# Optimization experiments

Hardware: AMD Instinct MI355X
Metric: run time of the kernel (lower is better)

## Reference

```python
import jax, jax.numpy as jnp
import numpy as np

LOG_STD_MAX = 2.0
LOG_STD_MIN = -5.0
N_LAYERS = 10
HID = 512
OBS = 21
ACT = 8
OVERALL = HID * (N_LAYERS + 1)          # 5632
IN_DIM = OBS + OVERALL                   # 5653
OUT_DIM = OVERALL + ACT                  # 5640
BATCH = 8192


def _block_banded_weight(rng):
    # staircase partitions, exactly as layer_init
    in_d = [0, OBS] + [OBS + HID * i for i in range(1, N_LAYERS + 2)]
    out_d = [0] + [HID * i for i in range(1, N_LAYERS + 2)] + [OUT_DIM]
    W = np.zeros((OUT_DIM, IN_DIM), dtype=np.float32)
    for i in range(N_LAYERS + 2):
        r0, r1 = out_d[i], out_d[i + 1]
        c0, c1 = in_d[i], in_d[i + 1]
        fan_in = c1 - c0
        std = np.sqrt(2.0 / fan_in)  # kaiming_normal_ fan_in, gain sqrt(2)
        W[r0:r1, c0:c1] = rng.standard_normal((r1 - r0, c1 - c0)).astype(np.float32) * std
    return jnp.asarray(W)


def setup_inputs() -> dict:
    key = jax.random.key(0)
    k1, k2, k3, k4, k5, k6 = jax.random.split(key, 6)
    rng = np.random.default_rng(0)
    return {
        "obs": jax.random.normal(k1, (BATCH, OBS), dtype=jnp.float32),
        "hidden0": jax.random.uniform(k2, (BATCH, OVERALL), dtype=jnp.float32),
        "prev_mean": jax.random.normal(k3, (BATCH, ACT), dtype=jnp.float32),
        "prev_logstd": jax.random.normal(k4, (BATCH, ACT), dtype=jnp.float32),
        "W_mean": _block_banded_weight(rng),
        "b_mean": jnp.zeros((OUT_DIM,), dtype=jnp.float32),
        "W_logstd": jax.random.normal(k5, (ACT, IN_DIM), dtype=jnp.float32) / np.sqrt(IN_DIM),
        "b_logstd": jax.random.normal(k6, (ACT,), dtype=jnp.float32) * 0.01,
    }


def reference(obs, hidden0, prev_mean, prev_logstd, W_mean, b_mean, W_logstd, b_logstd):
    x = jnp.concatenate([obs, hidden0], axis=1)            # [B, IN_DIM]
    new_x = x @ W_mean.T + b_mean                          # [B, OUT_DIM]
    new_hidden = jax.nn.relu(new_x[:, :-ACT])              # [B, OVERALL]
    new_mean = new_x[:, -ACT:]                             # [B, ACT]
    new_log_std = x @ W_logstd.T + b_logstd                # [B, ACT]
    # outputs come from the PREVIOUS step's (mean, log_std)
    log_std = jnp.tanh(prev_logstd)
    log_std = LOG_STD_MIN + 0.5 * (LOG_STD_MAX - LOG_STD_MIN) * (log_std + 1.0)
    return (prev_mean, log_std, new_hidden, new_mean, new_log_std)
```

## Files before the change

### kernel.cpp

```cpp
#include <hip/hip_runtime.h>
#include <math.h>

typedef unsigned short u16;
typedef unsigned int u32;
typedef __attribute__((ext_vector_type(8))) short short8;
typedef __attribute__((ext_vector_type(4))) float float4v;

#define BATCH   8192
#define OBS     21
#define HID     512
#define NL      10
#define OVERALL 5632
#define IN_DIM  5653
#define ACT     8

#define O_PM   0
#define O_LS   65536
#define O_NH   131072
#define O_NM   (131072 + BATCH*OVERALL)
#define O_NLS  (O_NM + 65536)

#define WSP_TOTAL (10*512*512)
#define WSP_BYTES ((size_t)WSP_TOTAL * 2)

__device__ __forceinline__ u16 f2bf(float f) {
    u32 u = __float_as_uint(f);
    u32 r = (u + 0x7fffu + ((u >> 16) & 1u)) >> 16;
    return (u16)r;
}
__device__ __forceinline__ u32 pkbf(float a, float b) {
    return (u32)f2bf(a) | ((u32)f2bf(b) << 16);
}
__device__ __forceinline__ void gload_lds16(const void* g, void* l) {
    __builtin_amdgcn_global_load_lds(
        (const __attribute__((address_space(1))) char*)g,
        (__attribute__((address_space(3))) char*)l, 16, 0, 0);
}

__global__ __launch_bounds__(256) void k_pack(const float* __restrict__ Wm,
                                              u16* __restrict__ ws) {
    int idx = blockIdx.x * 256 + threadIdx.x;
    if (idx >= WSP_TOTAL) return;
    int z = idx >> 18;
    int rem = idx & 262143;
    int n = rem >> 9, k = rem & 511;
    float v = Wm[(size_t)(512 * (z + 1) + n) * IN_DIM + OBS + 512 * z + k];
    ws[idx] = f2bf(v);
}

#define BM 128
#define BK 32
#define LDA 40
__global__ __launch_bounds__(1024, 4) void k_fused(
        const float* __restrict__ X,
        const float* __restrict__ Wm_raw,
        const u16* __restrict__ Wp,
        const float* __restrict__ Wls_raw,
        const float* __restrict__ b_mean,
        float* __restrict__ out_h,
        float* __restrict__ out_ls,
        float* __restrict__ out_mean,
        int packed) {
    __shared__ __attribute__((aligned(16))) u16 As[BM * LDA];
    __shared__ __attribute__((aligned(16))) u16 Bs[512 * 32];
    __shared__ __attribute__((aligned(16))) u16 Wt[16 * 520];
    u16* Wt2 = (u16*)Bs;

    int t = threadIdx.x;
    int w = t >> 6, lane = t & 63;
    int quad = lane >> 4, r16 = lane & 15;
    int gm = blockIdx.x * BM;
    int z = blockIdx.y;
    bool mainz = (z < 10);
    int wm = (w >> 3) * 64;
    int wn = (w & 7) * 64;

    {
        int n = t >> 7;
        int k4 = (t & 127) * 4;
        const float* wr = Wls_raw + (size_t)n * IN_DIM + OBS + z * 512 + k4;
        u16* dst = &Wt[n * 520 + k4];
        dst[0] = f2bf(wr[0]); dst[1] = f2bf(wr[1]);
        dst[2] = f2bf(wr[2]); dst[3] = f2bf(wr[3]);
        if (!mainz) {
            const float* wr2 = Wm_raw + (size_t)(OVERALL + n) * IN_DIM + OBS + z * 512 + k4;
            u16* d2 = &Wt2[n * 520 + k4];
            d2[0] = f2bf(wr2[0]); d2[1] = f2bf(wr2[1]);
            d2[2] = f2bf(wr2[2]); d2[3] = f2bf(wr2[3]);
        }
    }

    int arow = t >> 3;
    int acol = (t & 7) * 4;
    const float* gA = X + (size_t)(gm + arow) * OVERALL + (size_t)z * 512 + acol;
    float4 areg = *(const float4*)(gA);

    float4v acc[4][4];
#pragma unroll
    for (int i = 0; i < 4; i++)
#pragma unroll
        for (int j = 0; j < 4; j++) acc[i][j] = (float4v)0.f;
    float4v accL = (float4v)0.f;

    for (int it = 0; it < 16; ++it) {
        int k0 = it * BK;
        __syncthreads();
        {
            uint2 p;
            p.x = pkbf(areg.x, areg.y);
            p.y = pkbf(areg.z, areg.w);
            *(uint2*)&As[arow * LDA + acol] = p;
        }
        if (mainz) {
            if (packed) {
#pragma unroll
                for (int i2 = 0; i2 < 2; ++i2) {
                    int base_row = i2 * 256 + w * 16;
                    int row = base_row + (lane >> 2);
                    int slot = lane & 3;
                    int j = (slot - row) & 3;
                    const u16* g = Wp + (size_t)z * 262144 + (size_t)row * 512 + k0 + j * 8;
                    gload_lds16(g, (char*)Bs + base_row * 64);
                }
            } else {
#pragma unroll
                for (int i2 = 0; i2 < 2; ++i2) {
                    int row = i2 * 256 + w * 16 + (lane >> 2);
                    int slot = lane & 3;
                    int j = (slot - row) & 3;
                    const float* g = Wm_raw + (size_t)(512 * (z + 1) + row) * IN_DIM
                                     + OBS + (size_t)z * 512 + k0 + j * 8;
                    uint4 q;
                    q.x = pkbf(g[0], g[1]); q.y = pkbf(g[2], g[3]);
                    q.z = pkbf(g[4], g[5]); q.w = pkbf(g[6], g[7]);
                    *(uint4*)&Bs[row * 32 + slot * 8] = q;
                }
            }
        }
        __syncthreads();
        if (it < 15) areg = *(const float4*)(gA + (it + 1) * BK);

        if (mainz) {
            short8 bfr[4];
#pragma unroll
            for (int j = 0; j < 4; j++) {
                int n = wn + j * 16 + r16;
                int s = (quad + n) & 3;
                bfr[j] = *(const short8*)&Bs[n * 32 + s * 8];
            }
#pragma unroll
            for (int i2 = 0; i2 < 4; i2++) {
                short8 af = *(const short8*)&As[(wm + i2 * 16 + r16) * LDA + quad * 8];
#pragma unroll
                for (int j = 0; j < 4; j++)
                    acc[i2][j] = __builtin_amdgcn_mfma_f32_16x16x32_bf16(af, bfr[j], acc[i2][j], 0, 0, 0);
            }
        }
        if (w < 8) {
            short8 aL = *(const short8*)&As[(w * 16 + r16) * LDA + quad * 8];
            short8 bL = *(const short8*)&Wt[r16 * 520 + k0 + quad * 8];
            accL = __builtin_amdgcn_mfma_f32_16x16x32_bf16(aL, bL, accL, 0, 0, 0);
        } else if (!mainz) {
            short8 aL = *(const short8*)&As[((w - 8) * 16 + r16) * LDA + quad * 8];
            short8 bL = *(const short8*)&Wt2[r16 * 520 + k0 + quad * 8];
            accL = __builtin_amdgcn_mfma_f32_16x16x32_bf16(aL, bL, accL, 0, 0, 0);
        }
    }

    if (mainz) {
        int colblock = (z + 1) * 512;
#pragma unroll
        for (int j = 0; j < 4; j++) {
            int n_loc = wn + j * 16 + r16;
            float bias = b_mean[colblock + n_loc];
#pragma unroll
            for (int i2 = 0; i2 < 4; i2++) {
                int m0 = gm + wm + i2 * 16 + quad * 4;
#pragma unroll
                for (int r = 0; r < 4; r++) {
                    float v = acc[i2][j][r] + bias;
                    out_h[(size_t)(m0 + r) * OVERALL + colblock + n_loc] = fmaxf(v, 0.f);
                }
            }
        }
    }
    if (w < 8) {
        if (r16 < ACT) {
#pragma unroll
            for (int r = 0; r < 4; r++) {
                int row = gm + w * 16 + quad * 4 + r;
                atomicAdd(&out_ls[(size_t)row * ACT + r16], accL[r]);
            }
        }
    } else if (!mainz) {
        if (r16 < ACT) {
            float bias = b_mean[OVERALL + r16];
#pragma unroll
            for (int r = 0; r < 4; r++) {
                int row = gm + (w - 8) * 16 + quad * 4 + r;
                out_mean[(size_t)row * ACT + r16] = accL[r] + bias;
            }
        }
    }
}

#define B0_ROWS 32
__global__ __launch_bounds__(256) void k_block0(const float* __restrict__ obs,
                                                const float* __restrict__ Wm,
                                                const float* __restrict__ b_mean,
                                                float* __restrict__ out_h) {
    __shared__ float w0[OBS * 512];
    __shared__ float bias_s[512];
    __shared__ float obs_s[B0_ROWS * OBS];
    int t = threadIdx.x;
    int b0 = blockIdx.x * B0_ROWS;
    for (int i = t; i < OBS * 512; i += 256) {
        int n = i / OBS, k = i - n * OBS;
        w0[k * 512 + n] = Wm[(size_t)n * IN_DIM + k];
    }
    for (int i = t; i < 512; i += 256) bias_s[i] = b_mean[i];
    for (int i = t; i < B0_ROWS * OBS; i += 256) obs_s[i] = obs[(size_t)b0 * OBS + i];
    __syncthreads();

    int n0 = (t & 127) * 4;
    int rh = t >> 7;
#pragma unroll 4
    for (int r = 0; r < 16; r++) {
        int row = rh * 16 + r;
        float acc0 = bias_s[n0], acc1 = bias_s[n0 + 1];
        float acc2 = bias_s[n0 + 2], acc3 = bias_s[n0 + 3];
#pragma unroll
        for (int k = 0; k < OBS; k++) {
            float xo = obs_s[row * OBS + k];
            const float* wr = &w0[k * 512 + n0];
            acc0 += xo * wr[0]; acc1 += xo * wr[1];
            acc2 += xo * wr[2]; acc3 += xo * wr[3];
        }
        float4 o;
        o.x = fmaxf(acc0, 0.f); o.y = fmaxf(acc1, 0.f);
        o.z = fmaxf(acc2, 0.f); o.w = fmaxf(acc3, 0.f);
        *(float4*)&out_h[(size_t)(b0 + row) * OVERALL + n0] = o;
    }
}

__global__ __launch_bounds__(256) void k_finish(const float* __restrict__ obs,
                                                const float* __restrict__ Wls,
                                                const float* __restrict__ b_logstd,
                                                const float* __restrict__ pm,
                                                const float* __restrict__ pls,
                                                float* __restrict__ o_pm,
                                                float* __restrict__ o_lstd,
                                                float* __restrict__ o_nls) {
    __shared__ float wobs[ACT * OBS];
    __shared__ float bls[ACT];
    int t = threadIdx.x;
    if (t < ACT * OBS) wobs[t] = Wls[(size_t)(t / OBS) * IN_DIM + (t % OBS)];
    if (t < ACT) bls[t] = b_logstd[t];
    __syncthreads();
    int row = blockIdx.x * 256 + t;
    float ob[OBS];
#pragma unroll
    for (int k = 0; k < OBS; k++) ob[k] = obs[(size_t)row * OBS + k];
#pragma unroll
    for (int n = 0; n < ACT; n++) {
        float a = bls[n];
#pragma unroll
        for (int k = 0; k < OBS; k++) a += ob[k] * wobs[n * OBS + k];
        o_nls[(size_t)row * ACT + n] += a;
    }
    float4 p0 = *(const float4*)(pm + (size_t)row * ACT);
    float4 p1 = *(const float4*)(pm + (size_t)row * ACT + 4);
    *(float4*)(o_pm + (size_t)row * ACT) = p0;
    *(float4*)(o_pm + (size_t)row * ACT + 4) = p1;
    float4 l0 = *(const float4*)(pls + (size_t)row * ACT);
    float4 l1 = *(const float4*)(pls + (size_t)row * ACT + 4);
    float4 q0, q1;
    q0.x = -5.f + 3.5f * (tanhf(l0.x) + 1.f);
    q0.y = -5.f + 3.5f * (tanhf(l0.y) + 1.f);
    q0.z = -5.f + 3.5f * (tanhf(l0.z) + 1.f);
    q0.w = -5.f + 3.5f * (tanhf(l0.w) + 1.f);
    q1.x = -5.f + 3.5f * (tanhf(l1.x) + 1.f);
    q1.y = -5.f + 3.5f * (tanhf(l1.y) + 1.f);
    q1.z = -5.f + 3.5f * (tanhf(l1.z) + 1.f);
    q1.w = -5.f + 3.5f * (tanhf(l1.w) + 1.f);
    *(float4*)(o_lstd + (size_t)row * ACT) = q0;
    *(float4*)(o_lstd + (size_t)row * ACT + 4) = q1;
}

extern "C" void kernel_launch(void* const* d_in, const int* in_sizes, int n_in,
                              void* d_out, int out_size, void* d_ws, size_t ws_size,
                              hipStream_t stream) {
    const float* obs         = (const float*)d_in[0];
    const float* hidden0     = (const float*)d_in[1];
    const float* prev_mean   = (const float*)d_in[2];
    const float* prev_logstd = (const float*)d_in[3];
    const float* W_mean      = (const float*)d_in[4];
    const float* b_mean      = (const float*)d_in[5];
    const float* W_logstd    = (const float*)d_in[6];
    const float* b_logstd    = (const float*)d_in[7];

    float* out   = (float*)d_out;
    float* o_pm  = out + O_PM;
    float* o_ls  = out + O_LS;
    float* o_nh  = out + O_NH;
    float* o_nm  = out + O_NM;
    float* o_nls = out + O_NLS;
    u16*   ws    = (u16*)d_ws;

    int packed = (ws != nullptr && ws_size >= WSP_BYTES) ? 1 : 0;

    if (packed) {
        k_pack<<<(WSP_TOTAL + 255) / 256, 256, 0, stream>>>(W_mean, ws);
    }
    hipMemsetAsync(o_nls, 0, (size_t)BATCH * ACT * sizeof(float), stream);
    k_fused<<<dim3(BATCH / BM, NL + 1), 1024, 0, stream>>>(
        hidden0, W_mean, ws, W_logstd, b_mean, o_nh, o_nls, o_nm, packed);
    k_block0<<<BATCH / B0_ROWS, 256, 0, stream>>>(obs, W_mean, b_mean, o_nh);
    k_finish<<<BATCH / 256, 256, 0, stream>>>(obs, W_logstd, b_logstd,
                                              prev_mean, prev_logstd,
                                              o_pm, o_ls, o_nls);
}
```

Measured before the change: 453.8 us.

## Stage whole A tile in LDS once and stream B fragments straight from global

The fused GEMM kernel now uses 64-row blocks of 512 threads. Each block loads its full 64x512 A slab into XOR-swizzled LDS once, with a single barrier, instead of double-staging A and B through LDS every k-step. Each wave reads its B fragments directly from the packed bf16 weights in global/L2 and the log-std weights straight from global memory, which removes the per-iteration barriers. The cost is more blocks, twice the weight re-reads across M tiles, and B loads that depend on cache hits.

```diff
diff --git a/kernel.cpp b/kernel.cpp
--- a/kernel.cpp
+++ b/kernel.cpp
@@ -30,11 +30,6 @@
 }
 __device__ __forceinline__ u32 pkbf(float a, float b) {
     return (u32)f2bf(a) | ((u32)f2bf(b) << 16);
-}
-__device__ __forceinline__ void gload_lds16(const void* g, void* l) {
-    __builtin_amdgcn_global_load_lds(
-        (const __attribute__((address_space(1))) char*)g,
-        (__attribute__((address_space(3))) char*)l, 16, 0, 0);
 }
 
 __global__ __launch_bounds__(256) void k_pack(const float* __restrict__ Wm,
@@ -48,10 +43,8 @@
     ws[idx] = f2bf(v);
 }
 
-#define BM 128
-#define BK 32
-#define LDA 40
-__global__ __launch_bounds__(1024, 4) void k_fused(
+#define BM 64
+__global__ __launch_bounds__(512, 4) void k_fused(
         const float* __restrict__ X,
         const float* __restrict__ Wm_raw,
         const u16* __restrict__ Wp,
@@ -61,144 +54,126 @@
         float* __restrict__ out_ls,
         float* __restrict__ out_mean,
         int packed) {
-    __shared__ __attribute__((aligned(16))) u16 As[BM * LDA];
-    __shared__ __attribute__((aligned(16))) u16 Bs[512 * 32];
-    __shared__ __attribute__((aligned(16))) u16 Wt[16 * 520];
-    u16* Wt2 = (u16*)Bs;
-
-    int t = threadIdx.x;
-    int w = t >> 6, lane = t & 63;
-    int quad = lane >> 4, r16 = lane & 15;
-    int gm = blockIdx.x * BM;
-    int z = blockIdx.y;
-    bool mainz = (z < 10);
-    int wm = (w >> 3) * 64;
-    int wn = (w & 7) * 64;
+    __shared__ __attribute__((aligned(16))) u16 As[64 * 512];
+
+    const int t = threadIdx.x;
+    const int w = t >> 6, lane = t & 63;
+    const int quad = lane >> 4, r16 = lane & 15;
+    const int gm = blockIdx.x * BM;
+    const int z = blockIdx.y;
+    const bool mainz = (z < 10);
 
     {
-        int n = t >> 7;
-        int k4 = (t & 127) * 4;
-        const float* wr = Wls_raw + (size_t)n * IN_DIM + OBS + z * 512 + k4;
-        u16* dst = &Wt[n * 520 + k4];
-        dst[0] = f2bf(wr[0]); dst[1] = f2bf(wr[1]);
-        dst[2] = f2bf(wr[2]); dst[3] = f2bf(wr[3]);
-        if (!mainz) {
-            const float* wr2 = Wm_raw + (size_t)(OVERALL + n) * IN_DIM + OBS + z * 512 + k4;
-            u16* d2 = &Wt2[n * 520 + k4];
-            d2[0] = f2bf(wr2[0]); d2[1] = f2bf(wr2[1]);
-            d2[2] = f2bf(wr2[2]); d2[3] = f2bf(wr2[3]);
-        }
-    }
-
-    int arow = t >> 3;
-    int acol = (t & 7) * 4;
-    const float* gA = X + (size_t)(gm + arow) * OVERALL + (size_t)z * 512 + acol;
-    float4 areg = *(const float4*)(gA);
+        const float* xb = X + (size_t)gm * OVERALL + (size_t)z * 512;
+#pragma unroll
+        for (int u = 0; u < 8; ++u) {
+            int row = u * 8 + w;
+            const float* g = xb + (size_t)row * OVERALL + lane * 8;
+            float4 f0 = *(const float4*)g;
+            float4 f1 = *(const float4*)(g + 4);
+            uint4 p;
+            p.x = pkbf(f0.x, f0.y); p.y = pkbf(f0.z, f0.w);
+            p.z = pkbf(f1.x, f1.y); p.w = pkbf(f1.z, f1.w);
+            *(uint4*)&As[row * 512 + ((lane ^ w) << 3)] = p;
+        }
+    }
+    __syncthreads();
 
     float4v acc[4][4];
 #pragma unroll
-    for (int i = 0; i < 4; i++)
-#pragma unroll
-        for (int j = 0; j < 4; j++) acc[i][j] = (float4v)0.f;
-    float4v accL = (float4v)0.f;
-
+    for (int i = 0; i < 4; ++i)
+#pragma unroll
+        for (int j = 0; j < 4; ++j) acc[i][j] = (float4v)0.f;
+    float4v accE = (float4v)0.f;
+
+    const int n8 = r16 & 7;
+    const u16* bp = Wp + (size_t)z * 262144
+                       + (size_t)(w * 64 + r16) * 512 + quad * 8;
+    const float* gL = Wls_raw + (size_t)n8 * IN_DIM + OBS + z * 512 + quad * 8;
+    const float* gM = Wm_raw + (size_t)(OVERALL + n8) * IN_DIM + OBS + z * 512 + quad * 8;
+
+#pragma unroll 4
     for (int it = 0; it < 16; ++it) {
-        int k0 = it * BK;
-        __syncthreads();
-        {
-            uint2 p;
-            p.x = pkbf(areg.x, areg.y);
-            p.y = pkbf(areg.z, areg.w);
-            *(uint2*)&As[arow * LDA + acol] = p;
+        const int k0 = it * 32;
+        const int phys = ((it * 4 + quad) ^ (r16 & 7)) << 3;
+        short8 a[4];
+#pragma unroll
+        for (int i2 = 0; i2 < 4; ++i2) {
+            int row = i2 * 16 + r16;
+            a[i2] = *(const short8*)&As[row * 512 + phys];
         }
         if (mainz) {
+            short8 b[4];
             if (packed) {
 #pragma unroll
-                for (int i2 = 0; i2 < 2; ++i2) {
-                    int base_row = i2 * 256 + w * 16;
-                    int row = base_row + (lane >> 2);
-                    int slot = lane & 3;
-                    int j = (slot - row) & 3;
-                    const u16* g = Wp + (size_t)z * 262144 + (size_t)row * 512 + k0 + j * 8;
-                    gload_lds16(g, (char*)Bs + base_row * 64);
+                for (int j = 0; j < 4; ++j)
+                    b[j] = *(const short8*)(bp + j * 8192 + k0);
+            } else {
+#pragma unroll
+                for (int j = 0; j < 4; ++j) {
+                    const float* g = Wm_raw
+                        + (size_t)(512 * (z + 1) + w * 64 + j * 16 + r16) * IN_DIM
+                        + OBS + (size_t)z * 512 + k0 + quad * 8;
+                    union { short8 s; uint4 u; } cb;
+                    cb.u.x = pkbf(g[0], g[1]); cb.u.y = pkbf(g[2], g[3]);
+                    cb.u.z = pkbf(g[4], g[5]); cb.u.w = pkbf(g[6], g[7]);
+                    b[j] = cb.s;
                 }
-            } else {
-#pragma unroll
-                for (int i2 = 0; i2 < 2; ++i2) {
-                    int row = i2 * 256 + w * 16 + (lane >> 2);
-                    int slot = lane & 3;
-                    int j = (slot - row) & 3;
-                    const float* g = Wm_raw + (size_t)(512 * (z + 1) + row) * IN_DIM
-                                     + OBS + (size_t)z * 512 + k0 + j * 8;
-                    uint4 q;
-                    q.x = pkbf(g[0], g[1]); q.y = pkbf(g[2], g[3]);
-                    q.z = pkbf(g[4], g[5]); q.w = pkbf(g[6], g[7]);
-                    *(uint4*)&Bs[row * 32 + slot * 8] = q;
-                }
-            }
-        }
-        __syncthreads();
-        if (it < 15) areg = *(const float4*)(gA + (it + 1) * BK);
-
-        if (mainz) {
-            short8 bfr[4];
-#pragma unroll
-            for (int j = 0; j < 4; j++) {
-                int n = wn + j * 16 + r16;
-                int s = (quad + n) & 3;
-                bfr[j] = *(const short8*)&Bs[n * 32 + s * 8];
-            }
-#pragma unroll
-            for (int i2 = 0; i2 < 4; i2++) {
-                short8 af = *(const short8*)&As[(wm + i2 * 16 + r16) * LDA + quad * 8];
-#pragma unroll
-                for (int j = 0; j < 4; j++)
-                    acc[i2][j] = __builtin_amdgcn_mfma_f32_16x16x32_bf16(af, bfr[j], acc[i2][j], 0, 0, 0);
-            }
-        }
-        if (w < 8) {
-            short8 aL = *(const short8*)&As[(w * 16 + r16) * LDA + quad * 8];
-            short8 bL = *(const short8*)&Wt[r16 * 520 + k0 + quad * 8];
-            accL = __builtin_amdgcn_mfma_f32_16x16x32_bf16(aL, bL, accL, 0, 0, 0);
+            }
+#pragma unroll
+            for (int i2 = 0; i2 < 4; ++i2)
+#pragma unroll
+                for (int j = 0; j < 4; ++j)
+                    acc[i2][j] = __builtin_amdgcn_mfma_f32_16x16x32_bf16(
+                        a[i2], b[j], acc[i2][j], 0, 0, 0);
+        }
+        if (w < 4) {
+            const float* g = gL + k0;
+            union { short8 s; uint4 u; } ce;
+            ce.u.x = pkbf(g[0], g[1]); ce.u.y = pkbf(g[2], g[3]);
+            ce.u.z = pkbf(g[4], g[5]); ce.u.w = pkbf(g[6], g[7]);
+            accE = __builtin_amdgcn_mfma_f32_16x16x32_bf16(a[w], ce.s, accE, 0, 0, 0);
         } else if (!mainz) {
-            short8 aL = *(const short8*)&As[((w - 8) * 16 + r16) * LDA + quad * 8];
-            short8 bL = *(const short8*)&Wt2[r16 * 520 + k0 + quad * 8];
-            accL = __builtin_amdgcn_mfma_f32_16x16x32_bf16(aL, bL, accL, 0, 0, 0);
+            const float* g = gM + k0;
+            union { short8 s; uint4 u; } ce;
+            ce.u.x = pkbf(g[0], g[1]); ce.u.y = pkbf(g[2], g[3]);
+            ce.u.z = pkbf(g[4], g[5]); ce.u.w = pkbf(g[6], g[7]);
+            accE = __builtin_amdgcn_mfma_f32_16x16x32_bf16(a[w - 4], ce.s, accE, 0, 0, 0);
         }
     }
 
     if (mainz) {
         int colblock = (z + 1) * 512;
 #pragma unroll
-        for (int j = 0; j < 4; j++) {
-            int n_loc = wn + j * 16 + r16;
+        for (int j = 0; j < 4; ++j) {
+            int n_loc = w * 64 + j * 16 + r16;
             float bias = b_mean[colblock + n_loc];
 #pragma unroll
-            for (int i2 = 0; i2 < 4; i2++) {
-                int m0 = gm + wm + i2 * 16 + quad * 4;
-#pragma unroll
-                for (int r = 0; r < 4; r++) {
+            for (int i2 = 0; i2 < 4; ++i2) {
+                int m0 = gm + i2 * 16 + quad * 4;
+#pragma unroll
+                for (int r = 0; r < 4; ++r) {
                     float v = acc[i2][j][r] + bias;
                     out_h[(size_t)(m0 + r) * OVERALL + colblock + n_loc] = fmaxf(v, 0.f);
                 }
             }
         }
     }
-    if (w < 8) {
+    if (w < 4) {
         if (r16 < ACT) {
 #pragma unroll
-            for (int r = 0; r < 4; r++) {
+            for (int r = 0; r < 4; ++r) {
                 int row = gm + w * 16 + quad * 4 + r;
-                atomicAdd(&out_ls[(size_t)row * ACT + r16], accL[r]);
+                atomicAdd(&out_ls[(size_t)row * ACT + r16], accE[r]);
             }
         }
     } else if (!mainz) {
         if (r16 < ACT) {
             float bias = b_mean[OVERALL + r16];
 #pragma unroll
-            for (int r = 0; r < 4; r++) {
-                int row = gm + (w - 8) * 16 + quad * 4 + r;
-                out_mean[(size_t)row * ACT + r16] = accL[r] + bias;
+            for (int r = 0; r < 4; ++r) {
+                int row = gm + (w - 4) * 16 + quad * 4 + r;
+                out_mean[(size_t)row * ACT + r16] = accE[r] + bias;
             }
         }
     }
@@ -313,7 +288,7 @@
         k_pack<<<(WSP_TOTAL + 255) / 256, 256, 0, stream>>>(W_mean, ws);
     }
     hipMemsetAsync(o_nls, 0, (size_t)BATCH * ACT * sizeof(float), stream);
-    k_fused<<<dim3(BATCH / BM, NL + 1), 1024, 0, stream>>>(
+    k_fused<<<dim3(BATCH / BM, NL + 1), 512, 0, stream>>>(
         hidden0, W_mean, ws, W_logstd, b_mean, o_nh, o_nls, o_nm, packed);
     k_block0<<<BATCH / B0_ROWS, 256, 0, stream>>>(obs, W_mean, b_mean, o_nh);
     k_finish<<<BATCH / 256, 256, 0, stream>>>(obs, W_logstd, b_logstd,
```

After: 837.7 us. 1.85x slower.

## Double-buffer A/B LDS tiles in fused GEMM and change B swizzle

Applied to the files above, without the earlier changes.

The fused banded GEMM now keeps two LDS buffers for the A and B tiles. Each iteration stages the next k-slice while the current one feeds the MFMAs, so the loop needs one barrier instead of two. The B-tile swizzle becomes (r + r>>2)&3 to cut LDS bank conflicts on the B fragment reads. The cost is roughly double the A/B LDS footprint, which can reduce resident blocks per CU. The explicit vmcnt(0) wait at the end of each iteration also stalls on the A prefetch issued for the following step.

```diff
diff --git a/kernel.cpp b/kernel.cpp
--- a/kernel.cpp
+++ b/kernel.cpp
@@ -36,6 +36,7 @@
         (const __attribute__((address_space(1))) char*)g,
         (__attribute__((address_space(3))) char*)l, 16, 0, 0);
 }
+__device__ __forceinline__ int swz4(int r) { return (r + (r >> 2)) & 3; }
 
 __global__ __launch_bounds__(256) void k_pack(const float* __restrict__ Wm,
                                               u16* __restrict__ ws) {
@@ -61,10 +62,10 @@
         float* __restrict__ out_ls,
         float* __restrict__ out_mean,
         int packed) {
-    __shared__ __attribute__((aligned(16))) u16 As[BM * LDA];
-    __shared__ __attribute__((aligned(16))) u16 Bs[512 * 32];
+    __shared__ __attribute__((aligned(16))) u16 As[2][BM * LDA];
+    __shared__ __attribute__((aligned(16))) u16 Bs[2][512 * 32];
     __shared__ __attribute__((aligned(16))) u16 Wt[16 * 520];
-    u16* Wt2 = (u16*)Bs;
+    u16* Wt2 = (u16*)&Bs[0][0];
 
     int t = threadIdx.x;
     int w = t >> 6, lane = t & 63;
@@ -95,76 +96,90 @@
     const float* gA = X + (size_t)(gm + arow) * OVERALL + (size_t)z * 512 + acol;
     float4 areg = *(const float4*)(gA);
 
+    auto stageB = [&](int buf, int kk) {
+        if (packed) {
+#pragma unroll
+            for (int i2 = 0; i2 < 2; ++i2) {
+                int base_row = i2 * 256 + w * 16;
+                int row = base_row + (lane >> 2);
+                int slot = lane & 3;
+                int j = (slot - swz4(row)) & 3;
+                const u16* g = Wp + (size_t)z * 262144 + (size_t)row * 512 + kk + j * 8;
+                gload_lds16(g, (char*)&Bs[buf][0] + base_row * 64);
+            }
+        } else {
+#pragma unroll
+            for (int i2 = 0; i2 < 2; ++i2) {
+                int row = i2 * 256 + w * 16 + (lane >> 2);
+                int slot = lane & 3;
+                int j = (slot - swz4(row)) & 3;
+                const float* g = Wm_raw + (size_t)(512 * (z + 1) + row) * IN_DIM
+                                 + OBS + (size_t)z * 512 + kk + j * 8;
+                uint4 q;
+                q.x = pkbf(g[0], g[1]); q.y = pkbf(g[2], g[3]);
+                q.z = pkbf(g[4], g[5]); q.w = pkbf(g[6], g[7]);
+                *(uint4*)&Bs[buf][row * 32 + slot * 8] = q;
+            }
+        }
+    };
+
     float4v acc[4][4];
 #pragma unroll
     for (int i = 0; i < 4; i++)
 #pragma unroll
         for (int j = 0; j < 4; j++) acc[i][j] = (float4v)0.f;
-    float4v accL = (float4v)0.f;
-
+    float4v accE = (float4v)0.f;
+
+    {
+        uint2 p;
+        p.x = pkbf(areg.x, areg.y);
+        p.y = pkbf(areg.z, areg.w);
+        *(uint2*)&As[0][arow * LDA + acol] = p;
+    }
+    if (mainz) stageB(0, 0);
+    areg = *(const float4*)(gA + BK);
+    asm volatile("s_waitcnt vmcnt(0) lgkmcnt(0)" ::: "memory");
+    __builtin_amdgcn_s_barrier();
+
+#pragma unroll 4
     for (int it = 0; it < 16; ++it) {
-        int k0 = it * BK;
-        __syncthreads();
-        {
+        const int cur = it & 1;
+        const int k0 = it * BK;
+        if (it < 15) {
             uint2 p;
             p.x = pkbf(areg.x, areg.y);
             p.y = pkbf(areg.z, areg.w);
-            *(uint2*)&As[arow * LDA + acol] = p;
-        }
-        if (mainz) {
-            if (packed) {
-#pragma unroll
-                for (int i2 = 0; i2 < 2; ++i2) {
-                    int base_row = i2 * 256 + w * 16;
-                    int row = base_row + (lane >> 2);
-                    int slot = lane & 3;
-                    int j = (slot - row) & 3;
-                    const u16* g = Wp + (size_t)z * 262144 + (size_t)row * 512 + k0 + j * 8;
-                    gload_lds16(g, (char*)Bs + base_row * 64);
-                }
-            } else {
-#pragma unroll
-                for (int i2 = 0; i2 < 2; ++i2) {
-                    int row = i2 * 256 + w * 16 + (lane >> 2);
-                    int slot = lane & 3;
-                    int j = (slot - row) & 3;
-                    const float* g = Wm_raw + (size_t)(512 * (z + 1) + row) * IN_DIM
-                                     + OBS + (size_t)z * 512 + k0 + j * 8;
-                    uint4 q;
-                    q.x = pkbf(g[0], g[1]); q.y = pkbf(g[2], g[3]);
-                    q.z = pkbf(g[4], g[5]); q.w = pkbf(g[6], g[7]);
-                    *(uint4*)&Bs[row * 32 + slot * 8] = q;
-                }
-            }
-        }
-        __syncthreads();
-        if (it < 15) areg = *(const float4*)(gA + (it + 1) * BK);
-
+            *(uint2*)&As[cur ^ 1][arow * LDA + acol] = p;
+            if (mainz) stageB(cur ^ 1, k0 + BK);
+            if (it < 14) areg = *(const float4*)(gA + (it + 2) * BK);
+        }
         if (mainz) {
             short8 bfr[4];
 #pragma unroll
             for (int j = 0; j < 4; j++) {
                 int n = wn + j * 16 + r16;
-                int s = (quad + n) & 3;
-                bfr[j] = *(const short8*)&Bs[n * 32 + s * 8];
+                int s = (quad + swz4(n)) & 3;
+                bfr[j] = *(const short8*)&Bs[cur][n * 32 + s * 8];
             }
 #pragma unroll
             for (int i2 = 0; i2 < 4; i2++) {
-                short8 af = *(const short8*)&As[(wm + i2 * 16 + r16) * LDA + quad * 8];
+                short8 af = *(const short8*)&As[cur][(wm + i2 * 16 + r16) * LDA + quad * 8];
 #pragma unroll
                 for (int j = 0; j < 4; j++)
                     acc[i2][j] = __builtin_amdgcn_mfma_f32_16x16x32_bf16(af, bfr[j], acc[i2][j], 0, 0, 0);
             }
         }
         if (w < 8) {
-            short8 aL = *(const short8*)&As[(w * 16 + r16) * LDA + quad * 8];
+            short8 aL = *(const short8*)&As[cur][(w * 16 + r16) * LDA + quad * 8];
             short8 bL = *(const short8*)&Wt[r16 * 520 + k0 + quad * 8];
-            accL = __builtin_amdgcn_mfma_f32_16x16x32_bf16(aL, bL, accL, 0, 0, 0);
+            accE = __builtin_amdgcn_mfma_f32_16x16x32_bf16(aL, bL, accE, 0, 0, 0);
         } else if (!mainz) {
-            short8 aL = *(const short8*)&As[((w - 8) * 16 + r16) * LDA + quad * 8];
+            short8 aL = *(const short8*)&As[cur][((w - 8) * 16 + r16) * LDA + quad * 8];
             short8 bL = *(const short8*)&Wt2[r16 * 520 + k0 + quad * 8];
-            accL = __builtin_amdgcn_mfma_f32_16x16x32_bf16(aL, bL, accL, 0, 0, 0);
-        }
+            accE = __builtin_amdgcn_mfma_f32_16x16x32_bf16(aL, bL, accE, 0, 0, 0);
+        }
+        asm volatile("s_waitcnt vmcnt(0) lgkmcnt(0)" ::: "memory");
+        __builtin_amdgcn_s_barrier();
     }
 
     if (mainz) {
@@ -189,7 +204,7 @@
 #pragma unroll
             for (int r = 0; r < 4; r++) {
                 int row = gm + w * 16 + quad * 4 + r;
-                atomicAdd(&out_ls[(size_t)row * ACT + r16], accL[r]);
+                atomicAdd(&out_ls[(size_t)row * ACT + r16], accE[r]);
             }
         }
     } else if (!mainz) {
@@ -198,7 +213,7 @@
 #pragma unroll
             for (int r = 0; r < 4; r++) {
                 int row = gm + (w - 8) * 16 + quad * 4 + r;
-                out_mean[(size_t)row * ACT + r16] = accL[r] + bias;
+                out_mean[(size_t)row * ACT + r16] = accE[r] + bias;
             }
         }
     }
```

Measured after the change: 460.6 us. About the same (+1.5%).

## Halve batch tile to 64 rows with 512-thread blocks and new B swizzle

Applied to the files above, without the earlier changes.

Shrinks the fused GEMM block from 128 to 64 batch rows and from 16 to 8 waves, so each wave now covers all 64 rows against a 64-column slice. This doubles the grid size, which is meant to improve occupancy and load balance across CUs. The cost is that every block still loads the full 512x512 weight tile per z, so weight traffic per output row doubles. It also replaces the B-tile LDS swizzle with a new (r + r>>2)&3 rotation to reduce bank conflicts, and adjusts the logstd/mean side-GEMM wave mapping to match.

```diff
diff --git a/kernel.cpp b/kernel.cpp
--- a/kernel.cpp
+++ b/kernel.cpp
@@ -36,6 +36,7 @@
         (const __attribute__((address_space(1))) char*)g,
         (__attribute__((address_space(3))) char*)l, 16, 0, 0);
 }
+__device__ __forceinline__ int swz4(int r) { return (r + (r >> 2)) & 3; }
 
 __global__ __launch_bounds__(256) void k_pack(const float* __restrict__ Wm,
                                               u16* __restrict__ ws) {
@@ -48,10 +49,10 @@
     ws[idx] = f2bf(v);
 }
 
-#define BM 128
+#define BM 64
 #define BK 32
 #define LDA 40
-__global__ __launch_bounds__(1024, 4) void k_fused(
+__global__ __launch_bounds__(512, 4) void k_fused(
         const float* __restrict__ X,
         const float* __restrict__ Wm_raw,
         const u16* __restrict__ Wp,
@@ -72,21 +73,20 @@
     int gm = blockIdx.x * BM;
     int z = blockIdx.y;
     bool mainz = (z < 10);
-    int wm = (w >> 3) * 64;
-    int wn = (w & 7) * 64;
+    int wn = w * 64;
 
     {
-        int n = t >> 7;
-        int k4 = (t & 127) * 4;
-        const float* wr = Wls_raw + (size_t)n * IN_DIM + OBS + z * 512 + k4;
-        u16* dst = &Wt[n * 520 + k4];
-        dst[0] = f2bf(wr[0]); dst[1] = f2bf(wr[1]);
-        dst[2] = f2bf(wr[2]); dst[3] = f2bf(wr[3]);
+        int n = t >> 6;
+        int k8 = (t & 63) * 8;
+        const float* wr = Wls_raw + (size_t)n * IN_DIM + OBS + z * 512 + k8;
+        u16* dst = &Wt[n * 520 + k8];
+#pragma unroll
+        for (int q = 0; q < 8; ++q) dst[q] = f2bf(wr[q]);
         if (!mainz) {
-            const float* wr2 = Wm_raw + (size_t)(OVERALL + n) * IN_DIM + OBS + z * 512 + k4;
-            u16* d2 = &Wt2[n * 520 + k4];
-            d2[0] = f2bf(wr2[0]); d2[1] = f2bf(wr2[1]);
-            d2[2] = f2bf(wr2[2]); d2[3] = f2bf(wr2[3]);
+            const float* wr2 = Wm_raw + (size_t)(OVERALL + n) * IN_DIM + OBS + z * 512 + k8;
+            u16* d2 = &Wt2[n * 520 + k8];
+#pragma unroll
+            for (int q = 0; q < 8; ++q) d2[q] = f2bf(wr2[q]);
         }
     }
 
@@ -100,7 +100,7 @@
     for (int i = 0; i < 4; i++)
 #pragma unroll
         for (int j = 0; j < 4; j++) acc[i][j] = (float4v)0.f;
-    float4v accL = (float4v)0.f;
+    float4v accE = (float4v)0.f;
 
     for (int it = 0; it < 16; ++it) {
         int k0 = it * BK;
@@ -114,20 +114,20 @@
         if (mainz) {
             if (packed) {
 #pragma unroll
-                for (int i2 = 0; i2 < 2; ++i2) {
-                    int base_row = i2 * 256 + w * 16;
+                for (int i2 = 0; i2 < 4; ++i2) {
+                    int base_row = i2 * 128 + w * 16;
                     int row = base_row + (lane >> 2);
                     int slot = lane & 3;
-                    int j = (slot - row) & 3;
+                    int j = (slot - swz4(row)) & 3;
                     const u16* g = Wp + (size_t)z * 262144 + (size_t)row * 512 + k0 + j * 8;
                     gload_lds16(g, (char*)Bs + base_row * 64);
                 }
             } else {
 #pragma unroll
-                for (int i2 = 0; i2 < 2; ++i2) {
-                    int row = i2 * 256 + w * 16 + (lane >> 2);
+                for (int i2 = 0; i2 < 4; ++i2) {
+                    int row = i2 * 128 + w * 16 + (lane >> 2);
                     int slot = lane & 3;
-                    int j = (slot - row) & 3;
+                    int j = (slot - swz4(row)) & 3;
                     const float* g = Wm_raw + (size_t)(512 * (z + 1) + row) * IN_DIM
                                      + OBS + (size_t)z * 512 + k0 + j * 8;
                     uint4 q;
@@ -145,25 +145,25 @@
 #pragma unroll
             for (int j = 0; j < 4; j++) {
                 int n = wn + j * 16 + r16;
-                int s = (quad + n) & 3;
+                int s = (quad + swz4(n)) & 3;
                 bfr[j] = *(const short8*)&Bs[n * 32 + s * 8];
             }
 #pragma unroll
             for (int i2 = 0; i2 < 4; i2++) {
-                short8 af = *(const short8*)&As[(wm + i2 * 16 + r16) * LDA + quad * 8];
+                short8 af = *(const short8*)&As[(i2 * 16 + r16) * LDA + quad * 8];
 #pragma unroll
                 for (int j = 0; j < 4; j++)
                     acc[i2][j] = __builtin_amdgcn_mfma_f32_16x16x32_bf16(af, bfr[j], acc[i2][j], 0, 0, 0);
             }
         }
-        if (w < 8) {
+        if (w < 4) {
             short8 aL = *(const short8*)&As[(w * 16 + r16) * LDA + quad * 8];
             short8 bL = *(const short8*)&Wt[r16 * 520 + k0 + quad * 8];
-            accL = __builtin_amdgcn_mfma_f32_16x16x32_bf16(aL, bL, accL, 0, 0, 0);
+            accE = __builtin_amdgcn_mfma_f32_16x16x32_bf16(aL, bL, accE, 0, 0, 0);
         } else if (!mainz) {
-            short8 aL = *(const short8*)&As[((w - 8) * 16 + r16) * LDA + quad * 8];
+            short8 aL = *(const short8*)&As[((w - 4) * 16 + r16) * LDA + quad * 8];
             short8 bL = *(const short8*)&Wt2[r16 * 520 + k0 + quad * 8];
-            accL = __builtin_amdgcn_mfma_f32_16x16x32_bf16(aL, bL, accL, 0, 0, 0);
+            accE = __builtin_amdgcn_mfma_f32_16x16x32_bf16(aL, bL, accE, 0, 0, 0);
         }
     }
 
@@ -175,7 +175,7 @@
             float bias = b_mean[colblock + n_loc];
 #pragma unroll
             for (int i2 = 0; i2 < 4; i2++) {
-                int m0 = gm + wm + i2 * 16 + quad * 4;
+                int m0 = gm + i2 * 16 + quad * 4;
 #pragma unroll
                 for (int r = 0; r < 4; r++) {
                     float v = acc[i2][j][r] + bias;
@@ -184,12 +184,12 @@
             }
         }
     }
-    if (w < 8) {
+    if (w < 4) {
         if (r16 < ACT) {
 #pragma unroll
             for (int r = 0; r < 4; r++) {
                 int row = gm + w * 16 + quad * 4 + r;
-                atomicAdd(&out_ls[(size_t)row * ACT + r16], accL[r]);
+                atomicAdd(&out_ls[(size_t)row * ACT + r16], accE[r]);
             }
         }
     } else if (!mainz) {
@@ -197,8 +197,8 @@
             float bias = b_mean[OVERALL + r16];
 #pragma unroll
             for (int r = 0; r < 4; r++) {
-                int row = gm + (w - 8) * 16 + quad * 4 + r;
-                out_mean[(size_t)row * ACT + r16] = accL[r] + bias;
+                int row = gm + (w - 4) * 16 + quad * 4 + r;
+                out_mean[(size_t)row * ACT + r16] = accE[r] + bias;
             }
         }
     }
@@ -313,7 +313,7 @@
         k_pack<<<(WSP_TOTAL + 255) / 256, 256, 0, stream>>>(W_mean, ws);
     }
     hipMemsetAsync(o_nls, 0, (size_t)BATCH * ACT * sizeof(float), stream);
-    k_fused<<<dim3(BATCH / BM, NL + 1), 1024, 0, stream>>>(
+    k_fused<<<dim3(BATCH / BM, NL + 1), 512, 0, stream>>>(
         hidden0, W_mean, ws, W_logstd, b_mean, o_nh, o_nls, o_nm, packed);
     k_block0<<<BATCH / B0_ROWS, 256, 0, stream>>>(obs, W_mean, b_mean, o_nh);
     k_finish<<<BATCH / 256, 256, 0, stream>>>(obs, W_logstd, b_logstd,
```

Result: slower. 478.6 us (+5.4%).
